# Kernel tuning notes

Hardware: AMD Instinct MI355X
Metric: run time of the kernel (lower is better)

The kernel has to match this reference:

```python
import jax, jax.numpy as jnp
import numpy as np

B, N, EPG, FDIM, H = 128, 512, 4096, 128, 128
RATIO = 0.5
E = B * EPG
K1 = int(np.ceil(RATIO * N))      # 256
K2 = int(np.ceil(RATIO * K1))     # 128
K3 = int(np.ceil(RATIO * K2))     # 64


def setup_inputs():
    key = jax.random.key(0)
    ks = jax.random.split(key, 12)
    x = jax.random.normal(ks[0], (B * N, FDIM), jnp.float32)
    src = jax.random.randint(ks[1], (B, EPG), 0, N)
    dst = jax.random.randint(ks[2], (B, EPG), 0, N)
    off = (jnp.arange(B) * N)[:, None]
    edge_index = jnp.stack([(src + off).reshape(-1), (dst + off).reshape(-1)], 0).astype(jnp.int32)
    batch = (jnp.arange(B * N) // N).astype(jnp.int32)
    w = lambda k, s: jax.random.normal(k, s, jnp.float32) * 0.05
    return dict(
        x=x, edge_index=edge_index, batch=batch,
        W1=w(ks[3], (FDIM, H)), b1=jnp.zeros((H,), jnp.float32),
        Ws1=w(ks[4], (H, 1)), bs1=jnp.zeros((1,), jnp.float32),
        W2=w(ks[5], (H, H)), b2=jnp.zeros((H,), jnp.float32),
        Ws2=w(ks[6], (H, 1)), bs2=jnp.zeros((1,), jnp.float32),
        W3=w(ks[7], (H, H)), b3=jnp.zeros((H,), jnp.float32),
        Ws3=w(ks[8], (H, 1)), bs3=jnp.zeros((1,), jnp.float32))


def gcn(x, src, dst, emask, W, b):
    # PyG GCNConv: add self-loops, symmetric deg^-1/2 normalization.
    n = x.shape[0]
    h = x @ W
    deg = jnp.zeros((n,), x.dtype).at[dst].add(emask) + 1.0  # +1 for self-loop
    dinv = jax.lax.rsqrt(deg)
    norm = dinv[src] * dinv[dst] * emask                      # masked edges -> 0
    agg = jnp.zeros_like(h).at[dst].add(norm[:, None] * h[src])
    return agg + (dinv * dinv)[:, None] * h + b               # self-loop term + bias


def sag_pool(x, src, dst, emask, Ws, bs, n_per_graph, k):
    n_tot = x.shape[0]
    score = gcn(x, src, dst, emask, Ws, bs)[:, 0]
    sc = score.reshape(B, n_per_graph)
    topv, topi = jax.lax.top_k(sc, k)                         # [B,k] per-graph topk
    xg = x.reshape(B, n_per_graph, -1)
    xnew = jnp.take_along_axis(xg, topi[:, :, None], axis=1) * jnp.tanh(topv)[:, :, None]
    xnew = xnew.reshape(B * k, -1)
    perm = (topi + (jnp.arange(B) * n_per_graph)[:, None]).reshape(-1)
    newidx = jnp.full((n_tot,), -1, jnp.int32).at[perm].set(jnp.arange(B * k, dtype=jnp.int32))
    ns, nd = newidx[src], newidx[dst]
    valid = (ns >= 0) & (nd >= 0)
    emask_new = emask * valid.astype(x.dtype)                 # filter_adj via masking
    ns = jnp.where(valid, ns, 0)
    nd = jnp.where(valid, nd, 0)
    return xnew, ns, nd, emask_new


def readout(x, k):
    xg = x.reshape(B, k, -1)
    return jnp.concatenate([xg.max(axis=1), xg.mean(axis=1)], axis=1)  # [gmp, gap]


def reference(x, edge_index, batch, W1, b1, Ws1, bs1, W2, b2, Ws2, bs2, W3, b3, Ws3, bs3):
    src, dst = edge_index[0], edge_index[1]
    emask = jnp.ones((src.shape[0],), x.dtype)
    h = jax.nn.relu(gcn(x, src, dst, emask, W1, b1))
    h, src, dst, emask = sag_pool(h, src, dst, emask, Ws1, bs1, N, K1)
    x1 = readout(h, K1)
    h = jax.nn.relu(gcn(h, src, dst, emask, W2, b2))
    h, src, dst, emask = sag_pool(h, src, dst, emask, Ws2, bs2, K1, K2)
    x2 = readout(h, K2)
    h = jax.nn.relu(gcn(h, src, dst, emask, W3, b3))
    h, src, dst, emask = sag_pool(h, src, dst, emask, Ws3, bs3, K2, K3)
    x3 = readout(h, K3)
    return x1 + x2 + x3
```

## Files before the change

kernel.cpp:

```cpp
#include <hip/hip_runtime.h>
#include <math.h>

#define BGRAPH 128
#define ETOT   (128*4096)
#define EPG    4096
#define K1 256
#define K2 128
#define K3 64

__global__ __launch_bounds__(256) void gemm_tile2(const float* __restrict__ X,
                                                  const float* __restrict__ W,
                                                  float* __restrict__ Y){
  __shared__ float sA[32][132];
  __shared__ float sB[32][128];
  int t = threadIdx.x;
  int row0 = blockIdx.x * 128;
  int tx = t & 15;
  int ty = t >> 4;
  float acc[8][8];
  #pragma unroll
  for (int i = 0; i < 8; ++i)
    #pragma unroll
    for (int j = 0; j < 8; ++j) acc[i][j] = 0.f;

  for (int k0 = 0; k0 < 128; k0 += 32){
    #pragma unroll
    for (int i = 0; i < 4; ++i){
      int f = t + i*256;
      int row = f >> 3, c4 = f & 7;
      float4 v = *(const float4*)(X + (size_t)(row0 + row)*128 + k0 + c4*4);
      sA[c4*4+0][row] = v.x;
      sA[c4*4+1][row] = v.y;
      sA[c4*4+2][row] = v.z;
      sA[c4*4+3][row] = v.w;
    }
    #pragma unroll
    for (int i = 0; i < 4; ++i){
      int f = t + i*256;
      int kr = f >> 5, c4 = f & 31;
      *(float4*)&sB[kr][c4*4] = *(const float4*)(W + (size_t)(k0 + kr)*128 + c4*4);
    }
    __syncthreads();
    #pragma unroll
    for (int kk = 0; kk < 32; ++kk){
      float4 a0 = *(const float4*)&sA[kk][ty*8];
      float4 a1 = *(const float4*)&sA[kk][ty*8+4];
      float4 b0 = *(const float4*)&sB[kk][tx*8];
      float4 b1 = *(const float4*)&sB[kk][tx*8+4];
      float aa[8] = {a0.x,a0.y,a0.z,a0.w,a1.x,a1.y,a1.z,a1.w};
      float bb[8] = {b0.x,b0.y,b0.z,b0.w,b1.x,b1.y,b1.z,b1.w};
      #pragma unroll
      for (int i = 0; i < 8; ++i)
        #pragma unroll
        for (int j = 0; j < 8; ++j)
          acc[i][j] = fmaf(aa[i], bb[j], acc[i][j]);
    }
    __syncthreads();
  }
  #pragma unroll
  for (int i = 0; i < 8; ++i){
    float* yr = Y + (size_t)(row0 + ty*8 + i)*128 + tx*8;
    *(float4*)yr       = *(float4*)&acc[i][0];
    *(float4*)(yr + 4) = *(float4*)&acc[i][4];
  }
}

__global__ __launch_bounds__(1024) void scanfill_l1(const int* __restrict__ src,
    const int* __restrict__ dst, int* __restrict__ off, int* __restrict__ cnt,
    float* __restrict__ dinv, int* __restrict__ csr, float* __restrict__ coef){
  __shared__ int sc[512], sp[512], cur[512];
  __shared__ float sdv[512];
  __shared__ int ss[EPG], sd[EPG];
  int g = blockIdx.x, t = threadIdx.x;
  if (t < 512) sc[t] = 0;
  __syncthreads();
  const int* sg = src + g*EPG;
  const int* dg = dst + g*EPG;
  for (int e = t; e < EPG; e += 1024){
    int s = sg[e], d = dg[e];
    ss[e] = s; sd[e] = d;
    atomicAdd(&sc[d & 511], 1);
  }
  __syncthreads();
  int v = 0; float dv = 0.f;
  if (t < 512){
    v = sc[t];
    dv = rsqrtf((float)v + 1.f);
    sdv[t] = dv;
    dinv[g*512 + t] = dv;
    cnt[g*512 + t] = v;
    sp[t] = v;
  }
  __syncthreads();
  for (int d = 1; d < 512; d <<= 1){
    int u = 0;
    if (t >= d && t < 512) u = sp[t-d];
    __syncthreads();
    if (t < 512) sp[t] += u;
    __syncthreads();
  }
  if (t < 512){
    int pre = sp[t] - v;
    off[g*512 + t] = g*EPG + pre;
    sc[t] = pre;
    cur[t] = 0;
  }
  __syncthreads();
  int* cg = csr + g*EPG;
  float* cf = coef + g*EPG;
  for (int e = t; e < EPG; e += 1024){
    int s = ss[e], dl = sd[e] & 511;
    int slot = sc[dl] + atomicAdd(&cur[dl], 1);
    cg[slot] = s;
    cf[slot] = sdv[s & 511] * sdv[dl];
  }
}

__global__ void gather_agg(const float* __restrict__ hx, const int* __restrict__ csr,
                           const float* __restrict__ coef,
                           const int* __restrict__ off, const int* __restrict__ cnt,
                           const float* __restrict__ dinv, const float* __restrict__ bias,
                           const float* __restrict__ Ws, float* __restrict__ out,
                           float* __restrict__ hs, int npg, int n){
  int bpg = npg >> 3;
  int x = blockIdx.x >> 3, r = blockIdx.x & 7;
  int pos = x % bpg, grp = x / bpg;
  int g = grp*8 + r;
  int t = threadIdx.x;
  int node = g*npg + pos*8 + (t >> 5);
  int fl = t & 31;
  float dd = dinv[node];
  int o = off[node], deg = cnt[node];
  const float4* rows = (const float4*)hx;
  float4 a0 = {0,0,0,0}, a1 = {0,0,0,0}, a2 = {0,0,0,0}, a3 = {0,0,0,0};
  int e = o, end = o + deg;
  for (; e + 3 < end; e += 4){
    int s0 = csr[e], s1 = csr[e+1], s2 = csr[e+2], s3 = csr[e+3];
    float c0 = coef[e], c1 = coef[e+1], c2 = coef[e+2], c3 = coef[e+3];
    float4 v0 = rows[(size_t)s0*32 + fl];
    float4 v1 = rows[(size_t)s1*32 + fl];
    float4 v2 = rows[(size_t)s2*32 + fl];
    float4 v3 = rows[(size_t)s3*32 + fl];
    a0.x=fmaf(c0,v0.x,a0.x); a0.y=fmaf(c0,v0.y,a0.y); a0.z=fmaf(c0,v0.z,a0.z); a0.w=fmaf(c0,v0.w,a0.w);
    a1.x=fmaf(c1,v1.x,a1.x); a1.y=fmaf(c1,v1.y,a1.y); a1.z=fmaf(c1,v1.z,a1.z); a1.w=fmaf(c1,v1.w,a1.w);
    a2.x=fmaf(c2,v2.x,a2.x); a2.y=fmaf(c2,v2.y,a2.y); a2.z=fmaf(c2,v2.z,a2.z); a2.w=fmaf(c2,v2.w,a2.w);
    a3.x=fmaf(c3,v3.x,a3.x); a3.y=fmaf(c3,v3.y,a3.y); a3.z=fmaf(c3,v3.z,a3.z); a3.w=fmaf(c3,v3.w,a3.w);
  }
  for (; e < end; ++e){
    int s0 = csr[e];
    float c0 = coef[e];
    float4 v0 = rows[(size_t)s0*32 + fl];
    a0.x=fmaf(c0,v0.x,a0.x); a0.y=fmaf(c0,v0.y,a0.y); a0.z=fmaf(c0,v0.z,a0.z); a0.w=fmaf(c0,v0.w,a0.w);
  }
  float4 own = rows[(size_t)node*32 + fl];
  float4 bv  = ((const float4*)bias)[fl];
  float d2 = dd*dd;
  float4 rr;
  rr.x = fmaxf(fmaf(d2, own.x, (a0.x+a1.x)+(a2.x+a3.x) + bv.x), 0.f);
  rr.y = fmaxf(fmaf(d2, own.y, (a0.y+a1.y)+(a2.y+a3.y) + bv.y), 0.f);
  rr.z = fmaxf(fmaf(d2, own.z, (a0.z+a1.z)+(a2.z+a3.z) + bv.z), 0.f);
  rr.w = fmaxf(fmaf(d2, own.w, (a0.w+a1.w)+(a2.w+a3.w) + bv.w), 0.f);
  ((float4*)(out + (size_t)node*128))[fl] = rr;
  float4 w = ((const float4*)Ws)[fl];
  float p = rr.x*w.x + rr.y*w.y + rr.z*w.z + rr.w*w.w;
  p += __shfl_xor(p, 16);
  p += __shfl_xor(p, 8);
  p += __shfl_xor(p, 4);
  p += __shfl_xor(p, 2);
  p += __shfl_xor(p, 1);
  if (fl == 0) hs[node] = p;
}

template<int NP, int K, int HASNEXT, int COMPACT>
__global__ __launch_bounds__(1024) void mega(
    const float* __restrict__ hs, const int* __restrict__ csr_in,
    const float* __restrict__ coef_in, const int* __restrict__ off_in,
    const int* __restrict__ cnt_in, const float* __restrict__ dinv_in,
    const float* __restrict__ bs, const float* __restrict__ Hm,
    float* __restrict__ xnew, float* __restrict__ out,
    const int* __restrict__ pes, const int* __restrict__ ped,
    const int* __restrict__ ecnt_in,
    int* __restrict__ off_o, int* __restrict__ cnt_o, float* __restrict__ dinv_o,
    int* __restrict__ csr_o, int* __restrict__ dst_o, float* __restrict__ coef_o,
    int* __restrict__ ecnt_o)
{
  constexpr int R   = 1024 / NP;
  constexpr int LNP = (NP == 512) ? 9 : ((NP == 256) ? 8 : 7);
  __shared__ float shs[NP];
  __shared__ float spart[1024];
  __shared__ float sv[NP];
  __shared__ int   si[NP];
  __shared__ int   lnew[NP];
  __shared__ int   lperm[K];
  __shared__ float ltanh[K];
  __shared__ float smx[1024], ssm[1024];
  __shared__ int   ss[EPG], sd[EPG];
  __shared__ int   sc[K], sp2[K], cur[K];
  __shared__ float sdvn[K];
  int g = blockIdx.x, t = threadIdx.x;

  if (t < NP){ shs[t] = hs[g*NP + t]; lnew[t] = -1; }
  __syncthreads();

  int n = t & (NP-1);
  int p = t >> LNP;
  {
    int i = g*NP + n;
    int o = off_in[i], deg = cnt_in[i];
    float a = 0.f;
    for (int e = o + p; e < o + deg; e += R)
      a = fmaf(coef_in[e], shs[csr_in[e] & (NP-1)], a);
    spart[t] = a;
  }
  __syncthreads();
  float v = -INFINITY; int idx = n;
  if (p == 0){
    float a = spart[n];
    #pragma unroll
    for (int q = 1; q < R; ++q) a += spart[n + q*NP];
    float dd = dinv_in[g*NP + n];
    v = a + fmaf(dd*dd, shs[n], bs[0]);
  }
  #pragma unroll
  for (int ksz = 2; ksz <= NP; ksz <<= 1){
    #pragma unroll
    for (int j = ksz >> 1; j > 0; j >>= 1){
      float v2 = 0.f; int i2 = 0;
      if (j >= 64){
        __syncthreads();
        if (t < NP){ sv[t] = v; si[t] = idx; }
        __syncthreads();
        if (t < NP){ v2 = sv[t^j]; i2 = si[t^j]; }
      } else if (t < NP){
        v2 = __shfl_xor(v, j);
        i2 = __shfl_xor(idx, j);
      }
      if (t < NP){
        bool dir = ((t & ksz) == 0);
        bool pf = (v2 > v) || (v2 == v && i2 < idx);
        bool lower = (t & j) == 0;
        if (pf == (lower ? dir : !dir)){ v = v2; idx = i2; }
      }
    }
  }
  if (t < K){
    lperm[t] = idx;
    lnew[idx] = t;
    ltanh[t] = tanhf(v);
  }
  __syncthreads();

  {
    int f = t & 127, q = t >> 7;
    float mx = -INFINITY, sm = 0.f;
    for (int j = q; j < K; j += 8){
      float val = Hm[(size_t)(g*NP + lperm[j])*128 + f] * ltanh[j];
      xnew[(size_t)(g*K + j)*128 + f] = val;
      mx = fmaxf(mx, val); sm += val;
    }
    smx[t] = mx; ssm[t] = sm;
  }
  __syncthreads();
  if (t < 128){
    float mx = smx[t], sm = ssm[t];
    #pragma unroll
    for (int q = 1; q < 8; ++q){ mx = fmaxf(mx, smx[q*128+t]); sm += ssm[q*128+t]; }
    out[g*256 + t]       += mx;
    out[g*256 + 128 + t] += sm / (float)K;
  }
  if (!HASNEXT) return;
  __syncthreads();

  if (t < K) sc[t] = 0;
  __syncthreads();
  int E_in = COMPACT ? ecnt_in[g] : EPG;
  for (int e = t; e < E_in; e += 1024){
    int s = pes[g*EPG + e], d = ped[g*EPG + e];
    int rs = lnew[s & (NP-1)], rd = lnew[d & (NP-1)];
    bool ok = (rs | rd) >= 0;
    ss[e] = rs;
    sd[e] = ok ? rd : -1;
    if (ok) atomicAdd(&sc[rd], 1);
  }
  __syncthreads();
  int cv = 0; float dvn = 0.f;
  if (t < K){
    cv = sc[t];
    dvn = rsqrtf((float)cv + 1.f);
    sdvn[t] = dvn;
    dinv_o[g*K + t] = dvn;
    cnt_o[g*K + t] = cv;
    sp2[t] = cv;
  }
  __syncthreads();
  for (int d = 1; d < K; d <<= 1){
    int u = 0;
    if (t >= d && t < K) u = sp2[t-d];
    __syncthreads();
    if (t < K) sp2[t] += u;
    __syncthreads();
  }
  if (t < K){
    int pre = sp2[t] - cv;
    off_o[g*K + t] = g*EPG + pre;
    sc[t] = pre;
    cur[t] = 0;
    if (t == K-1) ecnt_o[g] = pre + cv;
  }
  __syncthreads();
  for (int e = t; e < E_in; e += 1024){
    int ndl = sd[e];
    if (ndl < 0) continue;
    int nsl = ss[e];
    int slot = sc[ndl] + atomicAdd(&cur[ndl], 1);
    csr_o[g*EPG + slot]  = g*K + nsl;
    dst_o[g*EPG + slot]  = g*K + ndl;
    coef_o[g*EPG + slot] = sdvn[nsl] * sdvn[ndl];
  }
}

extern "C" void kernel_launch(void* const* d_in, const int* in_sizes, int n_in,
                              void* d_out, int out_size, void* d_ws, size_t ws_size,
                              hipStream_t stream){
  const float* x0 = (const float*)d_in[0];
  const int*   ei = (const int*)d_in[1];
  const float* Wl[3]  = {(const float*)d_in[3], (const float*)d_in[7],  (const float*)d_in[11]};
  const float* bl[3]  = {(const float*)d_in[4], (const float*)d_in[8],  (const float*)d_in[12]};
  const float* Wsl[3] = {(const float*)d_in[5], (const float*)d_in[9],  (const float*)d_in[13]};
  const float* bsl[3] = {(const float*)d_in[6], (const float*)d_in[10], (const float*)d_in[14]};

  float* A     = (float*)d_ws;
  float* C     = A + (size_t)65536*128;
  float* D     = C + (size_t)65536*128;
  float* dinvA = D + (size_t)32768*128;
  float* dinvB = dinvA + 65536;
  float* hs    = dinvB + 65536;
  int* cntA    = (int*)(hs + 65536);
  int* cntB    = cntA + 65536;
  int* offA    = cntB + 65536;
  int* offB    = offA + 65536;
  int* csrA    = offB + 65536;
  int* csrB    = csrA + ETOT;
  int* dstA    = csrB + ETOT;
  int* dstB    = dstA + ETOT;
  float* coefA = (float*)(dstB + ETOT);
  float* coefB = coefA + ETOT;
  int* ecntA   = (int*)(coefB + ETOT);
  int* ecntB   = ecntA + 128;

  float* out = (float*)d_out;
  hipMemsetAsync(d_out, 0, (size_t)out_size*sizeof(float), stream);

  scanfill_l1<<<BGRAPH, 1024, 0, stream>>>(ei, ei + ETOT, offA, cntA, dinvA, csrA, coefA);
  gemm_tile2<<<65536/128, 256, 0, stream>>>(x0, Wl[0], A);
  gather_agg<<<65536/8, 256, 0, stream>>>(A, csrA, coefA, offA, cntA, dinvA, bl[0], Wsl[0], C, hs, 512, 65536);
  mega<512, K1, 1, 0><<<BGRAPH, 1024, 0, stream>>>(hs, csrA, coefA, offA, cntA, dinvA, bsl[0],
      C, D, out, ei, ei + ETOT, ecntA,
      offB, cntB, dinvB, csrB, dstB, coefB, ecntB);
  gemm_tile2<<<32768/128, 256, 0, stream>>>(D, Wl[1], A);
  gather_agg<<<32768/8, 256, 0, stream>>>(A, csrB, coefB, offB, cntB, dinvB, bl[1], Wsl[1], C, hs, 256, 32768);
  mega<256, K2, 1, 1><<<BGRAPH, 1024, 0, stream>>>(hs, csrB, coefB, offB, cntB, dinvB, bsl[1],
      C, D, out, csrB, dstB, ecntB,
      offA, cntA, dinvA, csrA, dstA, coefA, ecntA);
  gemm_tile2<<<16384/128, 256, 0, stream>>>(D, Wl[2], A);
  gather_agg<<<16384/8, 256, 0, stream>>>(A, csrA, coefA, offA, cntA, dinvA, bl[2], Wsl[2], C, hs, 128, 16384);
  mega<128, K3, 0, 1><<<BGRAPH, 1024, 0, stream>>>(hs, csrA, coefA, offA, cntA, dinvA, bsl[2],
      C, D, out, csrA, dstA, ecntA,
      offB, cntB, dinvB, csrB, dstB, coefB, ecntB);
}
```

Before: 190.1 us.

## Stage per-graph CSR edges in shared memory and drop output memset

scanfill_l1 now also writes a CSR-ordered destination array and the edge count, so every mega launch reads compacted CSR-order edges. mega stages csr/dst/coef for its graph into shared memory once and reuses them for both score aggregation and edge filtering, replacing scattered global reads. The first mega writes the readout instead of accumulating, which removes the memset. gather_agg also gains an 8-wide unrolled gather loop to put more loads in flight; the extra 16KB of shared memory in mega and higher register use are the trade-offs.

After: 190.0 us. About the same (-0.1%).

```diff
diff --git a/kernel.cpp b/kernel.cpp
--- a/kernel.cpp
+++ b/kernel.cpp
@@ -67,7 +67,8 @@
 
 __global__ __launch_bounds__(1024) void scanfill_l1(const int* __restrict__ src,
     const int* __restrict__ dst, int* __restrict__ off, int* __restrict__ cnt,
-    float* __restrict__ dinv, int* __restrict__ csr, float* __restrict__ coef){
+    float* __restrict__ dinv, int* __restrict__ csr, int* __restrict__ dsto,
+    float* __restrict__ coef, int* __restrict__ ecnt){
   __shared__ int sc[512], sp[512], cur[512];
   __shared__ float sdv[512];
   __shared__ int ss[EPG], sd[EPG];
@@ -105,14 +106,17 @@
     sc[t] = pre;
     cur[t] = 0;
   }
+  if (t == 0) ecnt[g] = EPG;
   __syncthreads();
   int* cg = csr + g*EPG;
+  int* dg2 = dsto + g*EPG;
   float* cf = coef + g*EPG;
   for (int e = t; e < EPG; e += 1024){
     int s = ss[e], dl = sd[e] & 511;
     int slot = sc[dl] + atomicAdd(&cur[dl], 1);
-    cg[slot] = s;
-    cf[slot] = sdv[s & 511] * sdv[dl];
+    cg[slot]  = s;
+    dg2[slot] = g*512 + dl;
+    cf[slot]  = sdv[s & 511] * sdv[dl];
   }
 }
 
@@ -134,17 +138,35 @@
   const float4* rows = (const float4*)hx;
   float4 a0 = {0,0,0,0}, a1 = {0,0,0,0}, a2 = {0,0,0,0}, a3 = {0,0,0,0};
   int e = o, end = o + deg;
+  for (; e + 7 < end; e += 8){
+    int sx[8]; float cx[8]; float4 vv[8];
+    #pragma unroll
+    for (int q = 0; q < 8; ++q){ sx[q] = csr[e+q]; cx[q] = coef[e+q]; }
+    #pragma unroll
+    for (int q = 0; q < 8; ++q) vv[q] = rows[(size_t)sx[q]*32 + fl];
+    #pragma unroll
+    for (int q = 0; q < 8; ++q){
+      float4& aq = (q&3)==0 ? a0 : ((q&3)==1 ? a1 : ((q&3)==2 ? a2 : a3));
+      aq.x = fmaf(cx[q], vv[q].x, aq.x);
+      aq.y = fmaf(cx[q], vv[q].y, aq.y);
+      aq.z = fmaf(cx[q], vv[q].z, aq.z);
+      aq.w = fmaf(cx[q], vv[q].w, aq.w);
+    }
+  }
   for (; e + 3 < end; e += 4){
-    int s0 = csr[e], s1 = csr[e+1], s2 = csr[e+2], s3 = csr[e+3];
-    float c0 = coef[e], c1 = coef[e+1], c2 = coef[e+2], c3 = coef[e+3];
-    float4 v0 = rows[(size_t)s0*32 + fl];
-    float4 v1 = rows[(size_t)s1*32 + fl];
-    float4 v2 = rows[(size_t)s2*32 + fl];
-    float4 v3 = rows[(size_t)s3*32 + fl];
-    a0.x=fmaf(c0,v0.x,a0.x); a0.y=fmaf(c0,v0.y,a0.y); a0.z=fmaf(c0,v0.z,a0.z); a0.w=fmaf(c0,v0.w,a0.w);
-    a1.x=fmaf(c1,v1.x,a1.x); a1.y=fmaf(c1,v1.y,a1.y); a1.z=fmaf(c1,v1.z,a1.z); a1.w=fmaf(c1,v1.w,a1.w);
-    a2.x=fmaf(c2,v2.x,a2.x); a2.y=fmaf(c2,v2.y,a2.y); a2.z=fmaf(c2,v2.z,a2.z); a2.w=fmaf(c2,v2.w,a2.w);
-    a3.x=fmaf(c3,v3.x,a3.x); a3.y=fmaf(c3,v3.y,a3.y); a3.z=fmaf(c3,v3.z,a3.z); a3.w=fmaf(c3,v3.w,a3.w);
+    int sx[4]; float cx[4]; float4 vv[4];
+    #pragma unroll
+    for (int q = 0; q < 4; ++q){ sx[q] = csr[e+q]; cx[q] = coef[e+q]; }
+    #pragma unroll
+    for (int q = 0; q < 4; ++q) vv[q] = rows[(size_t)sx[q]*32 + fl];
+    #pragma unroll
+    for (int q = 0; q < 4; ++q){
+      float4& aq = (q==0) ? a0 : ((q==1) ? a1 : ((q==2) ? a2 : a3));
+      aq.x = fmaf(cx[q], vv[q].x, aq.x);
+      aq.y = fmaf(cx[q], vv[q].y, aq.y);
+      aq.z = fmaf(cx[q], vv[q].z, aq.z);
+      aq.w = fmaf(cx[q], vv[q].w, aq.w);
+    }
   }
   for (; e < end; ++e){
     int s0 = csr[e];
@@ -171,14 +193,13 @@
   if (fl == 0) hs[node] = p;
 }
 
-template<int NP, int K, int HASNEXT, int COMPACT>
+template<int NP, int K, int HASNEXT, int FIRST>
 __global__ __launch_bounds__(1024) void mega(
     const float* __restrict__ hs, const int* __restrict__ csr_in,
-    const float* __restrict__ coef_in, const int* __restrict__ off_in,
-    const int* __restrict__ cnt_in, const float* __restrict__ dinv_in,
-    const float* __restrict__ bs, const float* __restrict__ Hm,
-    float* __restrict__ xnew, float* __restrict__ out,
-    const int* __restrict__ pes, const int* __restrict__ ped,
+    const int* __restrict__ dst_in, const float* __restrict__ coef_in,
+    const int* __restrict__ off_in, const int* __restrict__ cnt_in,
+    const float* __restrict__ dinv_in, const float* __restrict__ bs,
+    const float* __restrict__ Hm, float* __restrict__ xnew, float* __restrict__ out,
     const int* __restrict__ ecnt_in,
     int* __restrict__ off_o, int* __restrict__ cnt_o, float* __restrict__ dinv_o,
     int* __restrict__ csr_o, int* __restrict__ dst_o, float* __restrict__ coef_o,
@@ -186,6 +207,9 @@
 {
   constexpr int R   = 1024 / NP;
   constexpr int LNP = (NP == 512) ? 9 : ((NP == 256) ? 8 : 7);
+  __shared__ int   ss[EPG];
+  __shared__ int   sd[EPG];
+  __shared__ float scf[EPG];
   __shared__ float shs[NP];
   __shared__ float spart[1024];
   __shared__ float sv[NP];
@@ -194,22 +218,26 @@
   __shared__ int   lperm[K];
   __shared__ float ltanh[K];
   __shared__ float smx[1024], ssm[1024];
-  __shared__ int   ss[EPG], sd[EPG];
   __shared__ int   sc[K], sp2[K], cur[K];
   __shared__ float sdvn[K];
   int g = blockIdx.x, t = threadIdx.x;
+  int E_in = ecnt_in[g];
 
   if (t < NP){ shs[t] = hs[g*NP + t]; lnew[t] = -1; }
+  for (int e = t; e < E_in; e += 1024){
+    ss[e]  = csr_in[g*EPG + e];
+    sd[e]  = dst_in[g*EPG + e];
+    scf[e] = coef_in[g*EPG + e];
+  }
   __syncthreads();
 
   int n = t & (NP-1);
   int p = t >> LNP;
   {
-    int i = g*NP + n;
-    int o = off_in[i], deg = cnt_in[i];
+    int lo = off_in[g*NP + n] - g*EPG, deg = cnt_in[g*NP + n];
     float a = 0.f;
-    for (int e = o + p; e < o + deg; e += R)
-      a = fmaf(coef_in[e], shs[csr_in[e] & (NP-1)], a);
+    for (int e = lo + p; e < lo + deg; e += R)
+      a = fmaf(scf[e], shs[ss[e] & (NP-1)], a);
     spart[t] = a;
   }
   __syncthreads();
@@ -265,18 +293,21 @@
     float mx = smx[t], sm = ssm[t];
     #pragma unroll
     for (int q = 1; q < 8; ++q){ mx = fmaxf(mx, smx[q*128+t]); sm += ssm[q*128+t]; }
-    out[g*256 + t]       += mx;
-    out[g*256 + 128 + t] += sm / (float)K;
+    if (FIRST){
+      out[g*256 + t]       = mx;
+      out[g*256 + 128 + t] = sm / (float)K;
+    } else {
+      out[g*256 + t]       += mx;
+      out[g*256 + 128 + t] += sm / (float)K;
+    }
   }
   if (!HASNEXT) return;
   __syncthreads();
 
   if (t < K) sc[t] = 0;
   __syncthreads();
-  int E_in = COMPACT ? ecnt_in[g] : EPG;
   for (int e = t; e < E_in; e += 1024){
-    int s = pes[g*EPG + e], d = ped[g*EPG + e];
-    int rs = lnew[s & (NP-1)], rd = lnew[d & (NP-1)];
+    int rs = lnew[ss[e] & (NP-1)], rd = lnew[sd[e] & (NP-1)];
     bool ok = (rs | rd) >= 0;
     ss[e] = rs;
     sd[e] = ok ? rd : -1;
@@ -349,22 +380,18 @@
   int* ecntB   = ecntA + 128;
 
   float* out = (float*)d_out;
-  hipMemsetAsync(d_out, 0, (size_t)out_size*sizeof(float), stream);
-
-  scanfill_l1<<<BGRAPH, 1024, 0, stream>>>(ei, ei + ETOT, offA, cntA, dinvA, csrA, coefA);
+
+  scanfill_l1<<<BGRAPH, 1024, 0, stream>>>(ei, ei + ETOT, offA, cntA, dinvA, csrA, dstA, coefA, ecntA);
   gemm_tile2<<<65536/128, 256, 0, stream>>>(x0, Wl[0], A);
   gather_agg<<<65536/8, 256, 0, stream>>>(A, csrA, coefA, offA, cntA, dinvA, bl[0], Wsl[0], C, hs, 512, 65536);
-  mega<512, K1, 1, 0><<<BGRAPH, 1024, 0, stream>>>(hs, csrA, coefA, offA, cntA, dinvA, bsl[0],
-      C, D, out, ei, ei + ETOT, ecntA,
-      offB, cntB, dinvB, csrB, dstB, coefB, ecntB);
+  mega<512, K1, 1, 1><<<BGRAPH, 1024, 0, stream>>>(hs, csrA, dstA, coefA, offA, cntA, dinvA, bsl[0],
+      C, D, out, ecntA, offB, cntB, dinvB, csrB, dstB, coefB, ecntB);
   gemm_tile2<<<32768/128, 256, 0, stream>>>(D, Wl[1], A);
   gather_agg<<<32768/8, 256, 0, stream>>>(A, csrB, coefB, offB, cntB, dinvB, bl[1], Wsl[1], C, hs, 256, 32768);
-  mega<256, K2, 1, 1><<<BGRAPH, 1024, 0, stream>>>(hs, csrB, coefB, offB, cntB, dinvB, bsl[1],
-      C, D, out, csrB, dstB, ecntB,
-      offA, cntA, dinvA, csrA, dstA, coefA, ecntA);
+  mega<256, K2, 1, 0><<<BGRAPH, 1024, 0, stream>>>(hs, csrB, dstB, coefB, offB, cntB, dinvB, bsl[1],
+      C, D, out, ecntB, offA, cntA, dinvA, csrA, dstA, coefA, ecntA);
   gemm_tile2<<<16384/128, 256, 0, stream>>>(D, Wl[2], A);
   gather_agg<<<16384/8, 256, 0, stream>>>(A, csrA, coefA, offA, cntA, dinvA, bl[2], Wsl[2], C, hs, 128, 16384);
-  mega<128, K3, 0, 1><<<BGRAPH, 1024, 0, stream>>>(hs, csrA, coefA, offA, cntA, dinvA, bsl[2],
-      C, D, out, csrA, dstA, ecntA,
-      offB, cntB, dinvB, csrB, dstB, coefB, ecntB);
-}
+  mega<128, K3, 0, 0><<<BGRAPH, 1024, 0, stream>>>(hs, csrA, dstA, coefA, offA, cntA, dinvA, bsl[2],
+      C, D, out, ecntA, offB, cntB, dinvB, csrB, dstB, coefB, ecntB);
+}
```
